# Kernel tuning notes

Hardware: AMD Instinct MI355X
Metric: run time of the kernel (lower is better)

## Reference

```python
import jax, jax.numpy as jnp
import numpy as np

B, K, SD, NA = 2, 512, 60, 5
E, H, D, FF, NL = 256, 4, 64, 1024, 2
EPS_F = 1e-6   # feature_eps in phi(x)=relu(x)+eps
LN_EPS = 1e-5  # torch LayerNorm default eps


def setup_inputs() -> dict:
    key = jax.random.key(0)
    ks = jax.random.split(key, 16)
    f = lambda i, shape, s=0.02: jax.random.normal(ks[i], shape, dtype=jnp.float32) * s
    return {
        "rtg": jax.random.normal(ks[0], (B, K, 1), dtype=jnp.float32),
        "state": jax.random.normal(ks[1], (B, K, SD), dtype=jnp.float32),
        "action": jax.random.normal(ks[2], (B, K, NA), dtype=jnp.float32),
        "rtg_w": f(3, (1, E)), "rtg_b": jnp.zeros((E,), jnp.float32),
        "state_w": f(4, (SD, E)), "state_b": jnp.zeros((E,), jnp.float32),
        "action_w": f(5, (NA, E)), "action_b": jnp.zeros((E,), jnp.float32),
        "pos_emb": f(6, (K, E)),
        "norm1_g": jnp.ones((NL, E), jnp.float32), "norm1_b": jnp.zeros((NL, E), jnp.float32),
        "qkv_w": f(7, (NL, E, 3 * E)), "qkv_b": jnp.zeros((NL, 3 * E), jnp.float32),
        "out_w": f(8, (NL, E, E)), "out_b": jnp.zeros((NL, E), jnp.float32),
        "norm2_g": jnp.ones((NL, E), jnp.float32), "norm2_b": jnp.zeros((NL, E), jnp.float32),
        "ffn1_w": f(9, (NL, E, FF)), "ffn1_b": jnp.zeros((NL, FF), jnp.float32),
        "ffn2_w": f(10, (NL, FF, E)), "ffn2_b": jnp.zeros((NL, E), jnp.float32),
        "normf_g": jnp.ones((E,), jnp.float32), "normf_b": jnp.zeros((E,), jnp.float32),
        "pred_w": f(11, (E, NA)), "pred_b": jnp.zeros((NA,), jnp.float32),
    }


def _ln(x, g, b):
    m = x.mean(-1, keepdims=True)
    v = jnp.mean((x - m) ** 2, -1, keepdims=True)
    return (x - m) * jax.lax.rsqrt(v + LN_EPS) * g + b


def _attn(x, qkv_w, qkv_b, out_w, out_b):
    b, l, _ = x.shape
    qkv = (x @ qkv_w + qkv_b).reshape(b, l, 3, H, D).transpose(2, 0, 3, 1, 4)
    q, k, v = qkv[0], qkv[1], qkv[2]          # each (b,h,l,d)
    q = jax.nn.relu(q) + EPS_F
    k = jax.nn.relu(k) + EPS_F
    kv = jnp.cumsum(jnp.einsum('bhld,bhle->bhlde', k, v), axis=2)  # (b,h,l,d,e)
    kcum = jnp.cumsum(k, axis=2)
    num = jnp.einsum('bhld,bhlde->bhle', q, kv)
    den = jnp.maximum(jnp.einsum('bhld,bhld->bhl', q, kcum)[..., None], 1e-6)
    o = (num / den).transpose(0, 2, 1, 3).reshape(b, l, H * D)
    return o @ out_w + out_b


def reference(rtg, state, action, rtg_w, rtg_b, state_w, state_b, action_w, action_b,
              pos_emb, norm1_g, norm1_b, qkv_w, qkv_b, out_w, out_b,
              norm2_g, norm2_b, ffn1_w, ffn1_b, ffn2_w, ffn2_b,
              normf_g, normf_b, pred_w, pred_b):
    b, k, _ = state.shape
    p = pos_emb[:k][None]
    r = rtg @ rtg_w + rtg_b + p
    s = state @ state_w + state_b + p
    a = action @ action_w + action_b + p
    # interleave (r,s,a) per timestep -> (b, 3k, E)
    x = jnp.stack((r, s, a), axis=2).reshape(b, 3 * k, E)
    for i in range(NL):
        x = x + _attn(_ln(x, norm1_g[i], norm1_b[i]), qkv_w[i], qkv_b[i], out_w[i], out_b[i])
        h = _ln(x, norm2_g[i], norm2_b[i])
        h = jax.nn.gelu(h @ ffn1_w[i] + ffn1_b[i], approximate=False) @ ffn2_w[i] + ffn2_b[i]
        x = x + h
    x = _ln(x, normf_g, normf_b)
    return x[:, 1::3, :] @ pred_w + pred_b  # predict from state tokens -> (b,k,num_actions)
```

## Files before the change

kernel.cpp:

```cpp
#include <hip/hip_runtime.h>
#include <hip/hip_bf16.h>
#include <math.h>

#define B_  2
#define K_  512
#define SD_ 60
#define NA_ 5
#define E_  256
#define H_  4
#define D_  64
#define FF_ 1024
#define NL_ 2
#define L_  (3 * K_)
#define M_  (B_ * L_)
#define EPS_F 1e-6f
#define LN_EPS 1e-5f
#define CHK 64
#define NC_ (L_ / CHK)

using bf16x8 = __attribute__((ext_vector_type(8))) short;
using f32x4  = __attribute__((ext_vector_type(4))) float;
typedef unsigned short u16;

__device__ inline u16 f2b(float v) {
    __hip_bfloat16 h = __float2bfloat16(v);
    return *(u16*)&h;
}
__device__ inline float b2f(u16 v) {
    __hip_bfloat16 h = *(__hip_bfloat16*)&v;
    return __bfloat162float(h);
}

__global__ __launch_bounds__(256) void init_kernel(
    const float* __restrict__ qkv_w, const float* __restrict__ out_w,
    const float* __restrict__ ffn1_w, const float* __restrict__ ffn2_w,
    u16* __restrict__ qkvT, u16* __restrict__ outT,
    u16* __restrict__ f1T, u16* __restrict__ f2T,
    const float* __restrict__ rtg, const float* __restrict__ state,
    const float* __restrict__ action,
    const float* __restrict__ rtg_w, const float* __restrict__ rtg_b,
    const float* __restrict__ state_w, const float* __restrict__ state_b,
    const float* __restrict__ action_w, const float* __restrict__ action_b,
    const float* __restrict__ pos,
    const float* __restrict__ g, const float* __restrict__ bta,
    float* __restrict__ X, u16* __restrict__ Y)
{
    __shared__ u16 T[32][33];
    if (blockIdx.x < 1536) {
        int tb = blockIdx.x;
        int layer = tb / 768;
        int r = tb % 768;
        const float* src; u16* dst; int K, N, tidx;
        if (r < 192)      { src = qkv_w  + layer * 196608; dst = qkvT + layer * 196608; K = 256;  N = 768;  tidx = r; }
        else if (r < 256) { src = out_w  + layer * 65536;  dst = outT + layer * 65536;  K = 256;  N = 256;  tidx = r - 192; }
        else if (r < 512) { src = ffn1_w + layer * 262144; dst = f1T  + layer * 262144; K = 256;  N = 1024; tidx = r - 256; }
        else              { src = ffn2_w + layer * 262144; dst = f2T  + layer * 262144; K = 1024; N = 256;  tidx = r - 512; }
        int tilesN = N >> 5;
        int k0 = (tidx / tilesN) << 5;
        int n0 = (tidx % tilesN) << 5;
        int c = threadIdx.x & 31, r0 = threadIdx.x >> 5;
        for (int rr = r0; rr < 32; rr += 8)
            T[rr][c] = f2b(src[(size_t)(k0 + rr) * N + n0 + c]);
        __syncthreads();
        for (int rr = r0; rr < 32; rr += 8)
            dst[(size_t)(n0 + rr) * K + k0 + c] = T[c][rr];
        return;
    }
    int tok = (blockIdx.x - 1536) * 4 + (threadIdx.x >> 6);
    int lane = threadIdx.x & 63;
    int b = tok / L_, l = tok % L_;
    int j = l % 3, t = l / 3;
    int e0 = lane * 4;
    float4 val = *(const float4*)(pos + t * E_ + e0);
    if (j == 0) {
        float rv = rtg[b * K_ + t];
        float4 w = *(const float4*)(rtg_w + e0);
        float4 bb = *(const float4*)(rtg_b + e0);
        val.x += rv * w.x + bb.x; val.y += rv * w.y + bb.y;
        val.z += rv * w.z + bb.z; val.w += rv * w.w + bb.w;
    } else if (j == 1) {
        float4 a = *(const float4*)(state_b + e0);
        const float* srow = state + ((size_t)b * K_ + t) * SD_;
        for (int i = 0; i < SD_; i++) {
            float s = srow[i];
            float4 w = *(const float4*)(state_w + (size_t)i * E_ + e0);
            a.x += s * w.x; a.y += s * w.y; a.z += s * w.z; a.w += s * w.w;
        }
        val.x += a.x; val.y += a.y; val.z += a.z; val.w += a.w;
    } else {
        float4 a = *(const float4*)(action_b + e0);
        const float* arow = action + ((size_t)b * K_ + t) * NA_;
        #pragma unroll
        for (int i = 0; i < NA_; i++) {
            float s = arow[i];
            float4 w = *(const float4*)(action_w + (size_t)i * E_ + e0);
            a.x += s * w.x; a.y += s * w.y; a.z += s * w.z; a.w += s * w.w;
        }
        val.x += a.x; val.y += a.y; val.z += a.z; val.w += a.w;
    }
    *(float4*)(X + (size_t)tok * E_ + e0) = val;
    float s = val.x + val.y + val.z + val.w;
    #pragma unroll
    for (int o = 32; o; o >>= 1) s += __shfl_xor(s, o, 64);
    float mean = s * (1.f / E_);
    float dx = val.x - mean, dy = val.y - mean, dz = val.z - mean, dw = val.w - mean;
    float q = dx * dx + dy * dy + dz * dz + dw * dw;
    #pragma unroll
    for (int o = 32; o; o >>= 1) q += __shfl_xor(q, o, 64);
    float inv = rsqrtf(q * (1.f / E_) + LN_EPS);
    float4 gv = *(const float4*)(g + e0);
    float4 bv = *(const float4*)(bta + e0);
    ushort4 u;
    u.x = f2b(dx * inv * gv.x + bv.x); u.y = f2b(dy * inv * gv.y + bv.y);
    u.z = f2b(dz * inv * gv.z + bv.z); u.w = f2b(dw * inv * gv.w + bv.w);
    *(ushort4*)(Y + (size_t)tok * E_ + e0) = u;
}

template <int EPI>
__global__ __launch_bounds__(256) void mgemm(
    const u16* __restrict__ A, const u16* __restrict__ Bt,
    const float* __restrict__ bias,
    u16* __restrict__ C, int M, int N, int Kd)
{
    __shared__ __align__(16) u16 As[2][128 * 40];
    __shared__ __align__(16) u16 Bs[2][128 * 40];
    int tid = threadIdx.x;
    int bm = blockIdx.y * 128, bn = blockIdx.x * 128;
    int wave = tid >> 6, lane = tid & 63;
    int wm = (wave >> 1) * 64, wn = (wave & 1) * 64;
    int lr = lane & 15, kg = lane >> 4;

    int r0 = tid >> 2, g0 = (tid & 3) * 8;
    int r1 = r0 + 64;

    const u16* Ap0 = A + (size_t)(bm + r0) * Kd + g0;
    const u16* Ap1 = A + (size_t)(bm + r1) * Kd + g0;
    const u16* Bp0 = Bt + (size_t)(bn + r0) * Kd + g0;
    const u16* Bp1 = Bt + (size_t)(bn + r1) * Kd + g0;

    uint4 a0 = *(const uint4*)(Ap0);
    uint4 a1 = *(const uint4*)(Ap1);
    uint4 b0 = *(const uint4*)(Bp0);
    uint4 b1 = *(const uint4*)(Bp1);
    *(uint4*)&As[0][r0 * 40 + g0] = a0;
    *(uint4*)&As[0][r1 * 40 + g0] = a1;
    *(uint4*)&Bs[0][r0 * 40 + g0] = b0;
    *(uint4*)&Bs[0][r1 * 40 + g0] = b1;

    f32x4 acc[4][4] = {};
    int NT = Kd >> 5;
    for (int t = 0; t < NT; ++t) {
        int cur = t & 1;
        __syncthreads();
        if (t + 1 < NT) {
            int k1 = (t + 1) << 5;
            a0 = *(const uint4*)(Ap0 + k1);
            a1 = *(const uint4*)(Ap1 + k1);
            b0 = *(const uint4*)(Bp0 + k1);
            b1 = *(const uint4*)(Bp1 + k1);
        }
        bf16x8 af[4], bg[4];
        #pragma unroll
        for (int i = 0; i < 4; i++)
            af[i] = *(const bf16x8*)&As[cur][(wm + i * 16 + lr) * 40 + kg * 8];
        #pragma unroll
        for (int j = 0; j < 4; j++)
            bg[j] = *(const bf16x8*)&Bs[cur][(wn + j * 16 + lr) * 40 + kg * 8];
        #pragma unroll
        for (int i = 0; i < 4; i++)
            #pragma unroll
            for (int j = 0; j < 4; j++)
                acc[i][j] = __builtin_amdgcn_mfma_f32_16x16x32_bf16(
                    af[i], bg[j], acc[i][j], 0, 0, 0);
        if (t + 1 < NT) {
            *(uint4*)&As[cur ^ 1][r0 * 40 + g0] = a0;
            *(uint4*)&As[cur ^ 1][r1 * 40 + g0] = a1;
            *(uint4*)&Bs[cur ^ 1][r0 * 40 + g0] = b0;
            *(uint4*)&Bs[cur ^ 1][r1 * 40 + g0] = b1;
        }
    }

    #pragma unroll
    for (int i = 0; i < 4; i++) {
        #pragma unroll
        for (int j = 0; j < 4; j++) {
            int col = bn + wn + j * 16 + lr;
            float bc = bias[col];
            #pragma unroll
            for (int r = 0; r < 4; r++) {
                int row = bm + wm + i * 16 + kg * 4 + r;
                float v = acc[i][j][r] + bc;
                if (EPI == 1) v = 0.5f * v * (1.0f + erff(v * 0.70710678118654752f));
                if (EPI == 2) { if (col < 512) v = fmaxf(v, 0.f) + EPS_F; }
                C[(size_t)row * N + col] = f2b(v);
            }
        }
    }
}

template <int MODE>
__global__ __launch_bounds__(512) void gfuse64(
    const u16* __restrict__ A, const u16* __restrict__ Bt,
    const float* __restrict__ bias, float* __restrict__ X,
    const float* __restrict__ g, const float* __restrict__ bt,
    u16* __restrict__ Y, const float* __restrict__ W,
    const float* __restrict__ pb, float* __restrict__ Out, int Kd)
{
    __shared__ __align__(16) char smem[51200];
    u16* As = (u16*)smem;
    u16* Bs = (u16*)(smem + 10240);
    int tid = threadIdx.x;
    int bm = blockIdx.x * 64;
    int wave = tid >> 6, lane = tid & 63;
    int wr = wave >> 2, wc = wave & 3;
    int lr = lane & 15, kg = lane >> 4;

    int arow = tid >> 2, aq = (tid & 3) * 8;
    int brow = tid >> 1, bq = (tid & 1) * 16;

    const u16* Ap = A + (size_t)(bm + arow) * Kd + aq;
    const u16* Bp = Bt + (size_t)brow * Kd + bq;

    uint4 a0; uint4 b0, b1;
    if (tid < 256) a0 = *(const uint4*)(Ap);
    b0 = *(const uint4*)(Bp);
    b1 = *(const uint4*)(Bp + 8);
    if (tid < 256) *(uint4*)&As[arow * 40 + aq] = a0;
    *(uint4*)&Bs[brow * 40 + bq] = b0;
    *(uint4*)&Bs[brow * 40 + bq + 8] = b1;

    f32x4 acc[2][4] = {};
    int NT = Kd >> 5;
    for (int t = 0; t < NT; ++t) {
        int cur = t & 1;
        __syncthreads();
        if (t + 1 < NT) {
            int k1 = (t + 1) << 5;
            if (tid < 256) a0 = *(const uint4*)(Ap + k1);
            b0 = *(const uint4*)(Bp + k1);
            b1 = *(const uint4*)(Bp + k1 + 8);
        }
        bf16x8 af[2], bg[4];
        #pragma unroll
        for (int i = 0; i < 2; i++)
            af[i] = *(const bf16x8*)&As[cur * 2560 + (wr * 32 + i * 16 + lr) * 40 + kg * 8];
        #pragma unroll
        for (int j = 0; j < 4; j++)
            bg[j] = *(const bf16x8*)&Bs[cur * 10240 + (wc * 64 + j * 16 + lr) * 40 + kg * 8];
        #pragma unroll
        for (int i = 0; i < 2; i++)
            #pragma unroll
            for (int j = 0; j < 4; j++)
                acc[i][j] = __builtin_amdgcn_mfma_f32_16x16x32_bf16(
                    af[i], bg[j], acc[i][j], 0, 0, 0);
        if (t + 1 < NT) {
            if (tid < 256) *(uint4*)&As[(cur ^ 1) * 2560 + arow * 40 + aq] = a0;
            *(uint4*)&Bs[(cur ^ 1) * 10240 + brow * 40 + bq] = b0;
            *(uint4*)&Bs[(cur ^ 1) * 10240 + brow * 40 + bq + 8] = b1;
        }
    }
    __syncthreads();

    float* Xs = (float*)smem;
    int e0 = lane * 4;
    #pragma unroll
    for (int h = 0; h < 2; ++h) {
        if (wr == h) {
            #pragma unroll
            for (int j = 0; j < 4; j++) {
                int col = wc * 64 + j * 16 + lr;
                float bc = bias[col];
                #pragma unroll
                for (int i = 0; i < 2; i++) {
                    #pragma unroll
                    for (int rr = 0; rr < 4; rr++) {
                        int r32 = i * 16 + kg * 4 + rr;
                        float v = acc[i][j][rr] + bc
                                + X[(size_t)(bm + 32 * h + r32) * 256 + col];
                        Xs[r32 * 260 + col] = v;
                    }
                }
            }
        }
        __syncthreads();
        #pragma unroll
        for (int q = 0; q < 4; q++) {
            int r32 = wave * 4 + q;
            int gr = bm + 32 * h + r32;
            float4 v = *(const float4*)&Xs[r32 * 260 + e0];
            if (MODE == 1) {
                *(float4*)(X + (size_t)gr * 256 + e0) = v;
                float s = v.x + v.y + v.z + v.w;
                #pragma unroll
                for (int o = 32; o; o >>= 1) s += __shfl_xor(s, o, 64);
                float mean = s * (1.f / E_);
                float dx = v.x - mean, dy = v.y - mean, dz = v.z - mean, dw = v.w - mean;
                float qq = dx * dx + dy * dy + dz * dz + dw * dw;
                #pragma unroll
                for (int o = 32; o; o >>= 1) qq += __shfl_xor(qq, o, 64);
                float inv = rsqrtf(qq * (1.f / E_) + LN_EPS);
                float4 gv = *(const float4*)(g + e0);
                float4 bv = *(const float4*)(bt + e0);
                ushort4 u;
                u.x = f2b(dx * inv * gv.x + bv.x); u.y = f2b(dy * inv * gv.y + bv.y);
                u.z = f2b(dz * inv * gv.z + bv.z); u.w = f2b(dw * inv * gv.w + bv.w);
                *(ushort4*)(Y + (size_t)gr * 256 + e0) = u;
            } else {
                int b = gr / L_, l = gr % L_;
                if (l % 3 == 1) {
                    float s = v.x + v.y + v.z + v.w;
                    #pragma unroll
                    for (int o = 32; o; o >>= 1) s += __shfl_xor(s, o, 64);
                    float mean = s * (1.f / E_);
                    float dx = v.x - mean, dy = v.y - mean, dz = v.z - mean, dw = v.w - mean;
                    float qq = dx * dx + dy * dy + dz * dz + dw * dw;
                    #pragma unroll
                    for (int o = 32; o; o >>= 1) qq += __shfl_xor(qq, o, 64);
                    float inv = rsqrtf(qq * (1.f / E_) + LN_EPS);
                    float4 gv = *(const float4*)(g + e0);
                    float4 bv = *(const float4*)(bt + e0);
                    float y0 = dx * inv * gv.x + bv.x;
                    float y1 = dy * inv * gv.y + bv.y;
                    float y2 = dz * inv * gv.z + bv.z;
                    float y3 = dw * inv * gv.w + bv.w;
                    int si = b * K_ + l / 3;
                    #pragma unroll
                    for (int na = 0; na < NA_; na++) {
                        float a = y0 * W[(e0 + 0) * NA_ + na] + y1 * W[(e0 + 1) * NA_ + na]
                                + y2 * W[(e0 + 2) * NA_ + na] + y3 * W[(e0 + 3) * NA_ + na];
                        #pragma unroll
                        for (int o = 32; o; o >>= 1) a += __shfl_xor(a, o, 64);
                        if (lane == 0) Out[(size_t)si * NA_ + na] = a + pb[na];
                    }
                }
            }
        }
        __syncthreads();
    }
}

__global__ __launch_bounds__(256) void chunk_sum_kernel(
    const u16* __restrict__ QKV, float* __restrict__ S, float* __restrict__ Z)
{
    int blk = blockIdx.x;
    int c = blk % NC_;
    int bh = blk / NC_;
    int h = bh % H_;
    int b = bh / H_;
    __shared__ __align__(16) u16 Kt[64 * 72];
    __shared__ __align__(16) u16 Vt[64 * 72];
    int tid = threadIdx.x;
    const size_t base = ((size_t)b * L_ + (size_t)c * CHK) * 768 + h * 64;
    for (int i = tid; i < 1024; i += 256) {
        int t = i >> 4, d4 = (i & 15) << 2;
        ushort4 k = *(const ushort4*)(QKV + base + (size_t)t * 768 + 256 + d4);
        ushort4 v = *(const ushort4*)(QKV + base + (size_t)t * 768 + 512 + d4);
        Kt[(d4 + 0) * 72 + t] = k.x;
        Kt[(d4 + 1) * 72 + t] = k.y;
        Kt[(d4 + 2) * 72 + t] = k.z;
        Kt[(d4 + 3) * 72 + t] = k.w;
        Vt[(d4 + 0) * 72 + t] = v.x;
        Vt[(d4 + 1) * 72 + t] = v.y;
        Vt[(d4 + 2) * 72 + t] = v.z;
        Vt[(d4 + 3) * 72 + t] = v.w;
    }
    __syncthreads();
    int wave = tid >> 6, lane = tid & 63;
    int lr = lane & 15, kg = lane >> 4;
    int wm = wave * 16;
    bf16x8 a0 = *(const bf16x8*)&Kt[(wm + lr) * 72 + kg * 8];
    bf16x8 a1 = *(const bf16x8*)&Kt[(wm + lr) * 72 + 32 + kg * 8];
    f32x4 acc[4] = {};
    #pragma unroll
    for (int j = 0; j < 4; j++) {
        bf16x8 b0 = *(const bf16x8*)&Vt[(j * 16 + lr) * 72 + kg * 8];
        bf16x8 b1 = *(const bf16x8*)&Vt[(j * 16 + lr) * 72 + 32 + kg * 8];
        acc[j] = __builtin_amdgcn_mfma_f32_16x16x32_bf16(a0, b0, acc[j], 0, 0, 0);
        acc[j] = __builtin_amdgcn_mfma_f32_16x16x32_bf16(a1, b1, acc[j], 0, 0, 0);
    }
    if (tid < 64) {
        float z = 0.f;
        #pragma unroll 8
        for (int t = 0; t < 64; t++) z += b2f(Kt[tid * 72 + t]);
        Z[(size_t)blk * 64 + tid] = z;
    }
    float* Sp = S + (size_t)blk * 4096;
    #pragma unroll
    for (int j = 0; j < 4; j++) {
        #pragma unroll
        for (int rr = 0; rr < 4; rr++) {
            int d = wm + kg * 4 + rr;
            int e = j * 16 + lr;
            Sp[d * 64 + e] = acc[j][rr];
        }
    }
}

__global__ __launch_bounds__(256) void chunk_out_kernel(
    const u16* __restrict__ QKV, const float* __restrict__ S,
    const float* __restrict__ Z, u16* __restrict__ O)
{
    int blk = blockIdx.x;
    int c = blk % NC_;
    int bh = blk / NC_;
    int h = bh % H_;
    int b = bh / H_;
    __shared__ __align__(16) u16 Qb[64 * 72];
    __shared__ __align__(16) u16 Kb[64 * 72];
    __shared__ __align__(16) u16 Vt[64 * 72];
    __shared__ __align__(16) u16 KVt[64 * 72];
    __shared__ __align__(16) u16 Ps[64 * 72];
    __shared__ float kzs[64];
    __shared__ float rows[64];
    __shared__ float invs[64];
    int tid = threadIdx.x;
    const size_t base = ((size_t)b * L_ + (size_t)c * CHK) * 768 + h * 64;
    const float* Sbh = S + (size_t)bh * NC_ * 4096;
    for (int i = tid; i < 1024; i += 256) {
        int t = i >> 4, d4 = (i & 15) << 2;
        ushort4 q = *(const ushort4*)(QKV + base + (size_t)t * 768 + d4);
        ushort4 k = *(const ushort4*)(QKV + base + (size_t)t * 768 + 256 + d4);
        ushort4 v = *(const ushort4*)(QKV + base + (size_t)t * 768 + 512 + d4);
        *(ushort4*)&Qb[t * 72 + d4] = q;
        *(ushort4*)&Kb[t * 72 + d4] = k;
        Vt[(d4 + 0) * 72 + t] = v.x;
        Vt[(d4 + 1) * 72 + t] = v.y;
        Vt[(d4 + 2) * 72 + t] = v.z;
        Vt[(d4 + 3) * 72 + t] = v.w;
        int d = t, e4 = d4;
        float4 a = make_float4(0.f, 0.f, 0.f, 0.f);
        for (int cc = 0; cc < c; cc++) {
            float4 s4 = *(const float4*)(Sbh + (size_t)cc * 4096 + d * 64 + e4);
            a.x += s4.x; a.y += s4.y; a.z += s4.z; a.w += s4.w;
        }
        KVt[(e4 + 0) * 72 + d] = f2b(a.x);
        KVt[(e4 + 1) * 72 + d] = f2b(a.y);
        KVt[(e4 + 2) * 72 + d] = f2b(a.z);
        KVt[(e4 + 3) * 72 + d] = f2b(a.w);
    }
    if (tid < 64) {
        float z = 0.f;
        const float* Zbh = Z + (size_t)bh * NC_ * 64;
        for (int cc = 0; cc < c; cc++) z += Zbh[cc * 64 + tid];
        kzs[tid] = z;
    }
    __syncthreads();

    int wave = tid >> 6, lane = tid & 63;
    int lr = lane & 15, kg = lane >> 4;
    int wm = wave * 16;

    bf16x8 aq0 = *(const bf16x8*)&Qb[(wm + lr) * 72 + kg * 8];
    bf16x8 aq1 = *(const bf16x8*)&Qb[(wm + lr) * 72 + 32 + kg * 8];

    f32x4 accs[4] = {};
    #pragma unroll
    for (int j = 0; j < 4; j++) {
        bf16x8 b0 = *(const bf16x8*)&Kb[(j * 16 + lr) * 72 + kg * 8];
        bf16x8 b1 = *(const bf16x8*)&Kb[(j * 16 + lr) * 72 + 32 + kg * 8];
        accs[j] = __builtin_amdgcn_mfma_f32_16x16x32_bf16(aq0, b0, accs[j], 0, 0, 0);
        accs[j] = __builtin_amdgcn_mfma_f32_16x16x32_bf16(aq1, b1, accs[j], 0, 0, 0);
    }
    float rsum[4] = {0.f, 0.f, 0.f, 0.f};
    #pragma unroll
    for (int j = 0; j < 4; j++) {
        #pragma unroll
        for (int rr = 0; rr < 4; rr++) {
            int m = wm + kg * 4 + rr;
            int n = j * 16 + lr;
            float v = (n <= m) ? accs[j][rr] : 0.f;
            rsum[rr] += v;
            Ps[m * 72 + n] = f2b(v);
        }
    }
    #pragma unroll
    for (int rr = 0; rr < 4; rr++) {
        float s = rsum[rr];
        s += __shfl_xor(s, 1, 64);
        s += __shfl_xor(s, 2, 64);
        s += __shfl_xor(s, 4, 64);
        s += __shfl_xor(s, 8, 64);
        if (lr == 0) rows[wm + kg * 4 + rr] = s;
    }
    __syncthreads();

    if (tid < 64) {
        float den = rows[tid];
        float acc = 0.f;
        #pragma unroll 8
        for (int d = 0; d < 64; d++) acc += b2f(Qb[tid * 72 + d]) * kzs[d];
        invs[tid] = 1.f / fmaxf(den + acc, 1e-6f);
    }

    bf16x8 ap0 = *(const bf16x8*)&Ps[(wm + lr) * 72 + kg * 8];
    bf16x8 ap1 = *(const bf16x8*)&Ps[(wm + lr) * 72 + 32 + kg * 8];
    f32x4 accn[4] = {};
    #pragma unroll
    for (int j = 0; j < 4; j++) {
        bf16x8 b0 = *(const bf16x8*)&KVt[(j * 16 + lr) * 72 + kg * 8];
        bf16x8 b1 = *(const bf16x8*)&KVt[(j * 16 + lr) * 72 + 32 + kg * 8];
        accn[j] = __builtin_amdgcn_mfma_f32_16x16x32_bf16(aq0, b0, accn[j], 0, 0, 0);
        accn[j] = __builtin_amdgcn_mfma_f32_16x16x32_bf16(aq1, b1, accn[j], 0, 0, 0);
        bf16x8 c0 = *(const bf16x8*)&Vt[(j * 16 + lr) * 72 + kg * 8];
        bf16x8 c1 = *(const bf16x8*)&Vt[(j * 16 + lr) * 72 + 32 + kg * 8];
        accn[j] = __builtin_amdgcn_mfma_f32_16x16x32_bf16(ap0, c0, accn[j], 0, 0, 0);
        accn[j] = __builtin_amdgcn_mfma_f32_16x16x32_bf16(ap1, c1, accn[j], 0, 0, 0);
    }
    __syncthreads();

    u16* Op = O + ((size_t)b * L_ + (size_t)c * CHK) * E_ + h * 64;
    #pragma unroll
    for (int j = 0; j < 4; j++) {
        #pragma unroll
        for (int rr = 0; rr < 4; rr++) {
            int m = wm + kg * 4 + rr;
            int e = j * 16 + lr;
            Op[(size_t)m * E_ + e] = f2b(accn[j][rr] * invs[m]);
        }
    }
}

extern "C" void kernel_launch(void* const* d_in, const int* in_sizes, int n_in,
                              void* d_out, int out_size, void* d_ws, size_t ws_size,
                              hipStream_t stream) {
    const float* rtg      = (const float*)d_in[0];
    const float* state    = (const float*)d_in[1];
    const float* action   = (const float*)d_in[2];
    const float* rtg_w    = (const float*)d_in[3];
    const float* rtg_b    = (const float*)d_in[4];
    const float* state_w  = (const float*)d_in[5];
    const float* state_b  = (const float*)d_in[6];
    const float* action_w = (const float*)d_in[7];
    const float* action_b = (const float*)d_in[8];
    const float* pos_emb  = (const float*)d_in[9];
    const float* norm1_g  = (const float*)d_in[10];
    const float* norm1_b  = (const float*)d_in[11];
    const float* qkv_w    = (const float*)d_in[12];
    const float* qkv_b    = (const float*)d_in[13];
    const float* out_w    = (const float*)d_in[14];
    const float* out_b    = (const float*)d_in[15];
    const float* norm2_g  = (const float*)d_in[16];
    const float* norm2_b  = (const float*)d_in[17];
    const float* ffn1_w   = (const float*)d_in[18];
    const float* ffn1_b   = (const float*)d_in[19];
    const float* ffn2_w   = (const float*)d_in[20];
    const float* ffn2_b   = (const float*)d_in[21];
    const float* normf_g  = (const float*)d_in[22];
    const float* normf_b  = (const float*)d_in[23];
    const float* pred_w   = (const float*)d_in[24];
    const float* pred_b   = (const float*)d_in[25];
    float* out = (float*)d_out;

    float* ws = (float*)d_ws;
    float* x    = ws;
    float* S    = x + 786432;
    float* Z    = S + 786432;
    u16*   yb   = (u16*)(Z + 12288);
    u16*   qkvb = yb + 786432;
    u16*   att  = qkvb + 2359296;
    u16*   h1   = att + 786432;
    u16*   qkvT = h1 + 3145728;
    u16*   outT = qkvT + 393216;
    u16*   f1T  = outT + 131072;
    u16*   f2T  = f1T + 524288;

    init_kernel<<<2304, 256, 0, stream>>>(
        qkv_w, out_w, ffn1_w, ffn2_w, qkvT, outT, f1T, f2T,
        rtg, state, action, rtg_w, rtg_b, state_w, state_b,
        action_w, action_b, pos_emb, norm1_g, norm1_b, x, yb);

    for (int i = 0; i < NL_; i++) {
        mgemm<2><<<dim3(768 / 128, M_ / 128), 256, 0, stream>>>(
            yb, qkvT + (size_t)i * 196608, qkv_b + i * 768, qkvb,
            M_, 768, E_);
        chunk_sum_kernel<<<B_ * H_ * NC_, 256, 0, stream>>>(qkvb, S, Z);
        chunk_out_kernel<<<B_ * H_ * NC_, 256, 0, stream>>>(qkvb, S, Z, att);
        gfuse64<1><<<M_ / 64, 512, 0, stream>>>(
            att, outT + (size_t)i * 65536, out_b + i * E_, x,
            norm2_g + i * E_, norm2_b + i * E_, yb,
            nullptr, nullptr, nullptr, E_);
        mgemm<1><<<dim3(FF_ / 128, M_ / 128), 256, 0, stream>>>(
            yb, f1T + (size_t)i * 262144, ffn1_b + i * FF_, h1,
            M_, FF_, E_);
        if (i == 0)
            gfuse64<1><<<M_ / 64, 512, 0, stream>>>(
                h1, f2T, ffn2_b, x,
                norm1_g + E_, norm1_b + E_, yb,
                nullptr, nullptr, nullptr, FF_);
        else
            gfuse64<2><<<M_ / 64, 512, 0, stream>>>(
                h1, f2T + (size_t)1 * 262144, ffn2_b + E_, x,
                normf_g, normf_b, nullptr,
                pred_w, pred_b, out, FF_);
    }
}
```

Baseline: 302.0 us.

## Shrink fused residual+LayerNorm GEMM row tile to 16 rows for more blocks

Replaces the 64-row, 512-thread fused GEMM+residual+LayerNorm kernel with a 16-row, 256-thread variant. Each wave now computes a 16x64 slice of the full 256-wide output, and the epilogue finishes in a single pass. The grid grows from 48 to 192 blocks, so the output-projection and FFN2 GEMMs fill more of the GPU's compute units. In exchange every block reloads the whole weight matrix, which multiplies weight traffic through L2 by four, and each MFMA gets less reuse of its B fragment.

```diff
diff --git a/kernel.cpp b/kernel.cpp
--- a/kernel.cpp
+++ b/kernel.cpp
@@ -199,97 +199,105 @@
 }
 
 template <int MODE>
-__global__ __launch_bounds__(512) void gfuse64(
+__global__ __launch_bounds__(256) void gres16(
     const u16* __restrict__ A, const u16* __restrict__ Bt,
     const float* __restrict__ bias, float* __restrict__ X,
     const float* __restrict__ g, const float* __restrict__ bt,
     u16* __restrict__ Y, const float* __restrict__ W,
     const float* __restrict__ pb, float* __restrict__ Out, int Kd)
 {
-    __shared__ __align__(16) char smem[51200];
-    u16* As = (u16*)smem;
-    u16* Bs = (u16*)(smem + 10240);
+    __shared__ __align__(16) char smem[43520];
+    u16* AsB = (u16*)smem;
+    u16* BsB = (u16*)(smem + 2560);
     int tid = threadIdx.x;
-    int bm = blockIdx.x * 64;
+    int bm = blockIdx.x * 16;
     int wave = tid >> 6, lane = tid & 63;
-    int wr = wave >> 2, wc = wave & 3;
     int lr = lane & 15, kg = lane >> 4;
 
-    int arow = tid >> 2, aq = (tid & 3) * 8;
-    int brow = tid >> 1, bq = (tid & 1) * 16;
-
-    const u16* Ap = A + (size_t)(bm + arow) * Kd + aq;
-    const u16* Bp = Bt + (size_t)brow * Kd + bq;
-
-    uint4 a0; uint4 b0, b1;
-    if (tid < 256) a0 = *(const uint4*)(Ap);
-    b0 = *(const uint4*)(Bp);
-    b1 = *(const uint4*)(Bp + 8);
-    if (tid < 256) *(uint4*)&As[arow * 40 + aq] = a0;
-    *(uint4*)&Bs[brow * 40 + bq] = b0;
-    *(uint4*)&Bs[brow * 40 + bq + 8] = b1;
-
-    f32x4 acc[2][4] = {};
+    int arow = tid >> 2, ac8 = (tid & 3) * 8;
+    bool al = tid < 64;
+    int br = tid >> 2, bg8 = (tid & 3) * 8;
+
+    const u16* Ap = A + (size_t)(bm + arow) * Kd + ac8;
+    const u16* Bp = Bt + (size_t)br * Kd + bg8;
+
+    uint4 aR; uint4 bR[4];
+    if (al) aR = *(const uint4*)(Ap);
+    #pragma unroll
+    for (int q = 0; q < 4; q++) bR[q] = *(const uint4*)(Bp + (size_t)(64 * q) * Kd);
+    if (al) *(uint4*)&AsB[arow * 40 + ac8] = aR;
+    #pragma unroll
+    for (int q = 0; q < 4; q++) *(uint4*)&BsB[(br + 64 * q) * 40 + bg8] = bR[q];
+
+    f32x4 acc[4] = {};
     int NT = Kd >> 5;
     for (int t = 0; t < NT; ++t) {
         int cur = t & 1;
         __syncthreads();
         if (t + 1 < NT) {
             int k1 = (t + 1) << 5;
-            if (tid < 256) a0 = *(const uint4*)(Ap + k1);
-            b0 = *(const uint4*)(Bp + k1);
-            b1 = *(const uint4*)(Bp + k1 + 8);
-        }
-        bf16x8 af[2], bg[4];
-        #pragma unroll
-        for (int i = 0; i < 2; i++)
-            af[i] = *(const bf16x8*)&As[cur * 2560 + (wr * 32 + i * 16 + lr) * 40 + kg * 8];
+            if (al) aR = *(const uint4*)(Ap + k1);
+            #pragma unroll
+            for (int q = 0; q < 4; q++)
+                bR[q] = *(const uint4*)(Bp + (size_t)(64 * q) * Kd + k1);
+        }
+        bf16x8 af = *(const bf16x8*)&AsB[cur * 640 + lr * 40 + kg * 8];
+        bf16x8 bg[4];
         #pragma unroll
         for (int j = 0; j < 4; j++)
-            bg[j] = *(const bf16x8*)&Bs[cur * 10240 + (wc * 64 + j * 16 + lr) * 40 + kg * 8];
-        #pragma unroll
-        for (int i = 0; i < 2; i++)
+            bg[j] = *(const bf16x8*)&BsB[cur * 10240 + (wave * 64 + j * 16 + lr) * 40 + kg * 8];
+        #pragma unroll
+        for (int j = 0; j < 4; j++)
+            acc[j] = __builtin_amdgcn_mfma_f32_16x16x32_bf16(af, bg[j], acc[j], 0, 0, 0);
+        if (t + 1 < NT) {
+            if (al) *(uint4*)&AsB[(cur ^ 1) * 640 + arow * 40 + ac8] = aR;
             #pragma unroll
-            for (int j = 0; j < 4; j++)
-                acc[i][j] = __builtin_amdgcn_mfma_f32_16x16x32_bf16(
-                    af[i], bg[j], acc[i][j], 0, 0, 0);
-        if (t + 1 < NT) {
-            if (tid < 256) *(uint4*)&As[(cur ^ 1) * 2560 + arow * 40 + aq] = a0;
-            *(uint4*)&Bs[(cur ^ 1) * 10240 + brow * 40 + bq] = b0;
-            *(uint4*)&Bs[(cur ^ 1) * 10240 + brow * 40 + bq + 8] = b1;
+            for (int q = 0; q < 4; q++)
+                *(uint4*)&BsB[(cur ^ 1) * 10240 + (br + 64 * q) * 40 + bg8] = bR[q];
         }
     }
     __syncthreads();
 
     float* Xs = (float*)smem;
+    #pragma unroll
+    for (int j = 0; j < 4; j++) {
+        int col = wave * 64 + j * 16 + lr;
+        float bc = bias[col];
+        #pragma unroll
+        for (int rr = 0; rr < 4; rr++) {
+            int row = kg * 4 + rr;
+            float v = acc[j][rr] + bc + X[(size_t)(bm + row) * 256 + col];
+            Xs[row * 260 + col] = v;
+        }
+    }
+    __syncthreads();
+
     int e0 = lane * 4;
     #pragma unroll
-    for (int h = 0; h < 2; ++h) {
-        if (wr == h) {
+    for (int q = 0; q < 4; q++) {
+        int row = wave * 4 + q;
+        int gr = bm + row;
+        float4 v = *(const float4*)&Xs[row * 260 + e0];
+        if (MODE == 1) {
+            *(float4*)(X + (size_t)gr * 256 + e0) = v;
+            float s = v.x + v.y + v.z + v.w;
             #pragma unroll
-            for (int j = 0; j < 4; j++) {
-                int col = wc * 64 + j * 16 + lr;
-                float bc = bias[col];
-                #pragma unroll
-                for (int i = 0; i < 2; i++) {
-                    #pragma unroll
-                    for (int rr = 0; rr < 4; rr++) {
-                        int r32 = i * 16 + kg * 4 + rr;
-                        float v = acc[i][j][rr] + bc
-                                + X[(size_t)(bm + 32 * h + r32) * 256 + col];
-                        Xs[r32 * 260 + col] = v;
-                    }
-                }
-            }
-        }
-        __syncthreads();
-        #pragma unroll
-        for (int q = 0; q < 4; q++) {
-            int r32 = wave * 4 + q;
-            int gr = bm + 32 * h + r32;
-            float4 v = *(const float4*)&Xs[r32 * 260 + e0];
-            if (MODE == 1) {
-                *(float4*)(X + (size_t)gr * 256 + e0) = v;
+            for (int o = 32; o; o >>= 1) s += __shfl_xor(s, o, 64);
+            float mean = s * (1.f / E_);
+            float dx = v.x - mean, dy = v.y - mean, dz = v.z - mean, dw = v.w - mean;
+            float qq = dx * dx + dy * dy + dz * dz + dw * dw;
+            #pragma unroll
+            for (int o = 32; o; o >>= 1) qq += __shfl_xor(qq, o, 64);
+            float inv = rsqrtf(qq * (1.f / E_) + LN_EPS);
+            float4 gv = *(const float4*)(g + e0);
+            float4 bv = *(const float4*)(bt + e0);
+            ushort4 u;
+            u.x = f2b(dx * inv * gv.x + bv.x); u.y = f2b(dy * inv * gv.y + bv.y);
+            u.z = f2b(dz * inv * gv.z + bv.z); u.w = f2b(dw * inv * gv.w + bv.w);
+            *(ushort4*)(Y + (size_t)gr * 256 + e0) = u;
+        } else {
+            int b = gr / L_, l = gr % L_;
+            if (l % 3 == 1) {
                 float s = v.x + v.y + v.z + v.w;
                 #pragma unroll
                 for (int o = 32; o; o >>= 1) s += __shfl_xor(s, o, 64);
@@ -301,41 +309,21 @@
                 float inv = rsqrtf(qq * (1.f / E_) + LN_EPS);
                 float4 gv = *(const float4*)(g + e0);
                 float4 bv = *(const float4*)(bt + e0);
-                ushort4 u;
-                u.x = f2b(dx * inv * gv.x + bv.x); u.y = f2b(dy * inv * gv.y + bv.y);
-                u.z = f2b(dz * inv * gv.z + bv.z); u.w = f2b(dw * inv * gv.w + bv.w);
-                *(ushort4*)(Y + (size_t)gr * 256 + e0) = u;
-            } else {
-                int b = gr / L_, l = gr % L_;
-                if (l % 3 == 1) {
-                    float s = v.x + v.y + v.z + v.w;
+                float y0 = dx * inv * gv.x + bv.x;
+                float y1 = dy * inv * gv.y + bv.y;
+                float y2 = dz * inv * gv.z + bv.z;
+                float y3 = dw * inv * gv.w + bv.w;
+                int si = b * K_ + l / 3;
+                #pragma unroll
+                for (int na = 0; na < NA_; na++) {
+                    float a = y0 * W[(e0 + 0) * NA_ + na] + y1 * W[(e0 + 1) * NA_ + na]
+                            + y2 * W[(e0 + 2) * NA_ + na] + y3 * W[(e0 + 3) * NA_ + na];
                     #pragma unroll
-                    for (int o = 32; o; o >>= 1) s += __shfl_xor(s, o, 64);
-                    float mean = s * (1.f / E_);
-                    float dx = v.x - mean, dy = v.y - mean, dz = v.z - mean, dw = v.w - mean;
-                    float qq = dx * dx + dy * dy + dz * dz + dw * dw;
-                    #pragma unroll
-                    for (int o = 32; o; o >>= 1) qq += __shfl_xor(qq, o, 64);
-                    float inv = rsqrtf(qq * (1.f / E_) + LN_EPS);
-                    float4 gv = *(const float4*)(g + e0);
-                    float4 bv = *(const float4*)(bt + e0);
-                    float y0 = dx * inv * gv.x + bv.x;
-                    float y1 = dy * inv * gv.y + bv.y;
-                    float y2 = dz * inv * gv.z + bv.z;
-                    float y3 = dw * inv * gv.w + bv.w;
-                    int si = b * K_ + l / 3;
-                    #pragma unroll
-                    for (int na = 0; na < NA_; na++) {
-                        float a = y0 * W[(e0 + 0) * NA_ + na] + y1 * W[(e0 + 1) * NA_ + na]
-                                + y2 * W[(e0 + 2) * NA_ + na] + y3 * W[(e0 + 3) * NA_ + na];
-                        #pragma unroll
-                        for (int o = 32; o; o >>= 1) a += __shfl_xor(a, o, 64);
-                        if (lane == 0) Out[(size_t)si * NA_ + na] = a + pb[na];
-                    }
+                    for (int o = 32; o; o >>= 1) a += __shfl_xor(a, o, 64);
+                    if (lane == 0) Out[(size_t)si * NA_ + na] = a + pb[na];
                 }
             }
         }
-        __syncthreads();
     }
 }
 
@@ -575,7 +563,7 @@
             M_, 768, E_);
         chunk_sum_kernel<<<B_ * H_ * NC_, 256, 0, stream>>>(qkvb, S, Z);
         chunk_out_kernel<<<B_ * H_ * NC_, 256, 0, stream>>>(qkvb, S, Z, att);
-        gfuse64<1><<<M_ / 64, 512, 0, stream>>>(
+        gres16<1><<<M_ / 16, 256, 0, stream>>>(
             att, outT + (size_t)i * 65536, out_b + i * E_, x,
             norm2_g + i * E_, norm2_b + i * E_, yb,
             nullptr, nullptr, nullptr, E_);
@@ -583,12 +571,12 @@
             yb, f1T + (size_t)i * 262144, ffn1_b + i * FF_, h1,
             M_, FF_, E_);
         if (i == 0)
-            gfuse64<1><<<M_ / 64, 512, 0, stream>>>(
+            gres16<1><<<M_ / 16, 256, 0, stream>>>(
                 h1, f2T, ffn2_b, x,
                 norm1_g + E_, norm1_b + E_, yb,
                 nullptr, nullptr, nullptr, FF_);
         else
-            gfuse64<2><<<M_ / 64, 512, 0, stream>>>(
+            gres16<2><<<M_ / 16, 256, 0, stream>>>(
                 h1, f2T + (size_t)1 * 262144, ffn2_b + E_, x,
                 normf_g, normf_b, nullptr,
                 pred_w, pred_b, out, FF_);
```

Measured after the change: 342.4 us. 1.13x slower.
